# Performance work log

Hardware: AMD Instinct MI355X
Metric: run time of the kernel (lower is better)

## Reference

```python
import jax, jax.numpy as jnp
import numpy as np

NUM_CLASSES = 1024
KERNEL_MUL = 2.0
KERNEL_NUM = 5


def setup_inputs() -> dict:
    key = jax.random.key(0)
    k1, k2, k3 = jax.random.split(key, 3)
    N, D = 131072, 256
    x_rgb = jax.random.normal(k1, (N, D), dtype=jnp.float32)
    x_ir = jax.random.normal(k2, (N, D), dtype=jnp.float32)
    targets = jax.random.randint(k3, (N,), 0, NUM_CLASSES, dtype=jnp.int64)
    return {"x_rgb": x_rgb, "x_ir": x_ir, "targets": targets}


def _centers_by_id(x_rgb, x_ir, targets):
    # groupby-mean: one-pass segment sum + count (replaces the python loop)
    ones = jnp.ones(targets.shape, dtype=x_rgb.dtype)
    counts = jax.ops.segment_sum(ones, targets, num_segments=NUM_CLASSES)
    denom = jnp.maximum(counts, 1.0)[:, None]
    c_rgb = jax.ops.segment_sum(x_rgb, targets, num_segments=NUM_CLASSES) / denom
    c_ir = jax.ops.segment_sum(x_ir, targets, num_segments=NUM_CLASSES) / denom
    return c_rgb, c_ir  # [C, D] each


def _gaussian_kernel(total):
    # pairwise squared distances via ||a||^2 + ||b||^2 - 2 a.b (no NxNxD tensor)
    sq = jnp.sum(total * total, axis=1)
    dists = sq[:, None] + sq[None, :] - 2.0 * (total @ total.T)
    dists = jnp.maximum(dists, 0.0)  # fp-safety; exact form is nonnegative
    n = total.shape[0]
    # bandwidth computed on detached dists (matches `dists.data`)
    bandwidth = jax.lax.stop_gradient(jnp.sum(dists)) / (n * n - n)
    bandwidth = bandwidth / (KERNEL_MUL ** (KERNEL_NUM // 2))
    kernels = sum(
        jnp.exp(-dists / (bandwidth * (KERNEL_MUL ** i))) for i in range(KERNEL_NUM)
    )
    return kernels


def reference(x_rgb, x_ir, targets):
    c_rgb, c_ir = _centers_by_id(x_rgb, x_ir, targets)
    B = c_rgb.shape[0]
    total = jnp.concatenate([c_rgb, c_ir], axis=0)  # [2C, D]
    kernels = _gaussian_kernel(total)
    XX = kernels[:B, :B]
    YY = kernels[B:, B:]
    XY = kernels[:B, B:]
    YX = kernels[B:, :B]
    loss = jnp.mean(XX + YY - XY - YX)
    return loss
```

## Files before the change

### kernel.cpp

```cpp
#include <hip/hip_runtime.h>

#define NCLS 1024
#define DIM  256
#define NTOT 2048
#define CAP  256

__device__ __forceinline__ float4 f4add(float4 a, float4 b){
  return make_float4(a.x+b.x, a.y+b.y, a.z+b.z, a.w+b.w);
}

__global__ void k_init(int* cursor){
  cursor[threadIdx.x] = 0;
}

__global__ __launch_bounds__(256) void k_scatter(const int* __restrict__ tgt, int n,
                                                 int* __restrict__ cursor,
                                                 int* __restrict__ index){
  for (int i = blockIdx.x*blockDim.x + threadIdx.x; i < n; i += gridDim.x*blockDim.x){
    int t = tgt[i];
    int pos = atomicAdd(&cursor[t], 1);
    if (pos < CAP) index[t*CAP + pos] = i;
  }
}

__global__ __launch_bounds__(256) void k_gather(const float* __restrict__ xr,
    const float* __restrict__ xi, const int* __restrict__ index,
    const int* __restrict__ cursor, float* __restrict__ Ppart)
{
  int bid = blockIdx.x;
  int cls = bid >> 2;
  int h   = (bid >> 1) & 1;
  int a   = bid & 1;
  int tid = threadIdx.x;
  int l = tid & 63, g = tid >> 6;
  int cnt = cursor[cls]; if (cnt > CAP) cnt = CAP;
  int off = cls*CAP;
  int c0 = (cnt + 1) >> 1;
  int start = off + (h ? c0 : 0);
  int end   = off + (h ? cnt : c0);
  const float4* __restrict__ X4 = (const float4*)(a ? xi : xr);

  float4 s0 = make_float4(0,0,0,0), s1 = make_float4(0,0,0,0);
  int j = start + g;
  for (; j + 4 < end; j += 8){
    unsigned r0 = (unsigned)index[j];
    unsigned r1 = (unsigned)index[j+4];
    float4 v0 = X4[r0*64u + l];
    float4 v1 = X4[r1*64u + l];
    s0 = f4add(s0, v0);
    s1 = f4add(s1, v1);
  }
  if (j < end) s0 = f4add(s0, X4[(unsigned)index[j]*64u + l]);
  s0 = f4add(s0, s1);

  __shared__ float4 sh[256];
  sh[tid] = s0; __syncthreads();
  if (tid < 64){
    float4 r = f4add(f4add(sh[tid], sh[tid+64]), f4add(sh[tid+128], sh[tid+192]));
    ((float4*)Ppart)[bid*64 + tid] = r;
  }
}

__global__ __launch_bounds__(256) void k_combine(const float* __restrict__ Ppart,
    const int* __restrict__ cursor, float* __restrict__ T, float* __restrict__ sq)
{
  int wv  = blockIdx.x*4 + (threadIdx.x >> 6);
  int cls = wv >> 1, a = wv & 1;
  int l   = threadIdx.x & 63;
  const float4* P4 = (const float4*)Ppart;
  float4 p0 = P4[(cls*4 + 0 + a)*64 + l];
  float4 p1 = P4[(cls*4 + 2 + a)*64 + l];
  int cnt = cursor[cls]; if (cnt > CAP) cnt = CAP;
  float invd = 1.f / fmaxf((float)cnt, 1.f);
  float4 c;
  c.x = (p0.x + p1.x) * invd;
  c.y = (p0.y + p1.y) * invd;
  c.z = (p0.z + p1.z) * invd;
  c.w = (p0.w + p1.w) * invd;
  int row = a ? (NCLS + cls) : cls;
  ((float4*)T)[row*64 + l] = c;
  float v = c.x*c.x + c.y*c.y + c.z*c.z + c.w*c.w;
  #pragma unroll
  for (int o = 32; o > 0; o >>= 1) v += __shfl_down(v, o);
  if (l == 0) sq[row] = v;
}

__global__ __launch_bounds__(256) void k_colsum(const float* __restrict__ T,
                                                float* __restrict__ Pcol){
  int b = blockIdx.x;
  int tid = threadIdx.x;
  int l = tid & 63, g = tid >> 6;
  const float4* T4 = (const float4*)T;
  float4 acc = make_float4(0,0,0,0);
  for (int r = b*64 + g; r < b*64 + 64; r += 4)
    acc = f4add(acc, T4[r*64 + l]);
  __shared__ float4 sh[256];
  sh[tid] = acc; __syncthreads();
  if (tid < 64){
    float4 r = f4add(f4add(sh[tid], sh[tid+64]), f4add(sh[tid+128], sh[tid+192]));
    ((float4*)Pcol)[b*64 + tid] = r;
  }
}

__global__ __launch_bounds__(256) void k_bw(const float* __restrict__ sq,
    const float* __restrict__ Pcol, float* __restrict__ invbw,
    double* __restrict__ lossacc){
  int t = threadIdx.x;
  double acc = 0.0;
  for (int i = t; i < NTOT; i += 256) acc += (double)sq[i];
  float cs = 0.f;
  for (int b = 0; b < 32; ++b) cs += Pcol[b*DIM + t];
  double c2 = (double)cs * (double)cs;
  #pragma unroll
  for (int o = 32; o > 0; o >>= 1){
    acc += __shfl_down(acc, o);
    c2  += __shfl_down(c2, o);
  }
  __shared__ double ra[4], rc[4];
  int lane = t & 63, wid = t >> 6;
  if (lane == 0){ ra[wid] = acc; rc[wid] = c2; }
  __syncthreads();
  if (t == 0){
    double S_sq = ra[0]+ra[1]+ra[2]+ra[3];
    double S_cs = rc[0]+rc[1]+rc[2]+rc[3];
    double S1 = 2.0*(double)NTOT*S_sq - 2.0*S_cs;
    double bw = S1 / ((double)NTOT*(double)NTOT - (double)NTOT) / 4.0;
    #pragma unroll
    for (int k = 0; k < 5; ++k)
      invbw[k] = (float)(1.0 / (bw * (double)(1 << k)));
    *lossacc = 0.0;
  }
}

__global__ __launch_bounds__(256) void k_mmd(const float* __restrict__ T,
    const float* __restrict__ sq, const float* __restrict__ invbw,
    double* __restrict__ lossacc)
{
  int bx = blockIdx.x, by = blockIdx.y;
  if (bx < by) return;
  __shared__ float AsT[64][68];
  __shared__ float BsT[64][68];
  __shared__ float red[4];
  int tid = threadIdx.x;
  int tx = tid & 15, ty = tid >> 4;
  int rowA = by*64, rowB = bx*64;
  float acc[4][4];
  #pragma unroll
  for (int a = 0; a < 4; ++a)
    #pragma unroll
    for (int b = 0; b < 4; ++b) acc[a][b] = 0.f;

  for (int kk = 0; kk < DIM; kk += 64){
    #pragma unroll
    for (int it = 0; it < 4; ++it){
      int idx = it*256 + tid;
      int r = idx >> 4, c4 = idx & 15;
      float4 va = *(const float4*)&T[(rowA + r)*DIM + kk + c4*4];
      float4 vb = *(const float4*)&T[(rowB + r)*DIM + kk + c4*4];
      AsT[c4*4+0][r] = va.x; AsT[c4*4+1][r] = va.y;
      AsT[c4*4+2][r] = va.z; AsT[c4*4+3][r] = va.w;
      BsT[c4*4+0][r] = vb.x; BsT[c4*4+1][r] = vb.y;
      BsT[c4*4+2][r] = vb.z; BsT[c4*4+3][r] = vb.w;
    }
    __syncthreads();
    #pragma unroll 8
    for (int k = 0; k < 64; ++k){
      float4 av = *(const float4*)&AsT[k][ty*4];
      float4 bv = *(const float4*)&BsT[k][tx*4];
      acc[0][0] += av.x*bv.x; acc[0][1] += av.x*bv.y; acc[0][2] += av.x*bv.z; acc[0][3] += av.x*bv.w;
      acc[1][0] += av.y*bv.x; acc[1][1] += av.y*bv.y; acc[1][2] += av.y*bv.z; acc[1][3] += av.y*bv.w;
      acc[2][0] += av.z*bv.x; acc[2][1] += av.z*bv.y; acc[2][2] += av.z*bv.z; acc[2][3] += av.z*bv.w;
      acc[3][0] += av.w*bv.x; acc[3][1] += av.w*bv.y; acc[3][2] += av.w*bv.z; acc[3][3] += av.w*bv.w;
    }
    __syncthreads();
  }

  float i0 = invbw[0], i1 = invbw[1], i2 = invbw[2], i3 = invbw[3], i4 = invbw[4];
  float wgt = (bx > by) ? 2.f : 1.f;
  float lacc = 0.f;
  #pragma unroll
  for (int a = 0; a < 4; ++a){
    int i = rowA + ty*4 + a;
    float sqi  = sq[i];
    float sgnI = (i < NCLS) ? 1.f : -1.f;
    #pragma unroll
    for (int b = 0; b < 4; ++b){
      int j = rowB + tx*4 + b;
      float d = sqi + sq[j] - 2.f*acc[a][b];
      d = fmaxf(d, 0.f);
      float w = __expf(-d*i0) + __expf(-d*i1) + __expf(-d*i2) + __expf(-d*i3) + __expf(-d*i4);
      lacc += ((j < NCLS) ? sgnI : -sgnI) * w;
    }
  }
  lacc *= wgt;
  #pragma unroll
  for (int o = 32; o > 0; o >>= 1) lacc += __shfl_down(lacc, o);
  int lane = tid & 63, wid = tid >> 6;
  if (lane == 0) red[wid] = lacc;
  __syncthreads();
  if (tid == 0) atomicAdd(lossacc, (double)(red[0]+red[1]+red[2]+red[3]));
}

__global__ void k_final(const double* __restrict__ lossacc, float* __restrict__ out){
  out[0] = (float)(*lossacc * (1.0 / ((double)NCLS * (double)NCLS)));
}

extern "C" void kernel_launch(void* const* d_in, const int* in_sizes, int n_in,
                              void* d_out, int out_size, void* d_ws, size_t ws_size,
                              hipStream_t stream) {
  const float* xr  = (const float*)d_in[0];
  const float* xi  = (const float*)d_in[1];
  const int*   tgt = (const int*)d_in[2];
  float* out = (float*)d_out;
  int n = in_sizes[2];

  char* w = (char*)d_ws;
  int* cursor   = (int*)w;
  int* index    = cursor + NCLS;
  float* T      = (float*)(index + NCLS*CAP);
  float* sq     = T + NTOT*DIM;
  float* invbw  = sq + NTOT;
  double* lossd = (double*)(invbw + 8);
  float* Ppart  = (float*)(lossd + 1);
  float* Pcol   = Ppart + 4*NCLS*DIM;

  k_init<<<1, 1024, 0, stream>>>(cursor);
  k_scatter<<<256, 256, 0, stream>>>(tgt, n, cursor, index);
  k_gather<<<4*NCLS, 256, 0, stream>>>(xr, xi, index, cursor, Ppart);
  k_combine<<<NTOT/4, 256, 0, stream>>>(Ppart, cursor, T, sq);
  k_colsum<<<32, 256, 0, stream>>>(T, Pcol);
  k_bw<<<1, 256, 0, stream>>>(sq, Pcol, invbw, lossd);
  k_mmd<<<dim3(32, 32), 256, 0, stream>>>(T, sq, invbw, lossd);
  k_final<<<1, 1, 0, stream>>>(lossd, out);
}
```

Baseline: 135.1 us.

## Compute pairwise Gram tile with split-bf16 MFMA instead of scalar FP32 FMA

The combine kernel now also writes hi/lo bf16 splits of the centers matrix. The MMD kernel computes the 64x64 Gram tiles with three bf16 MFMA 16x16x32 products per k-step (hi*hi, hi*lo, lo*hi) in place of a scalar FP32 outer-product loop. This moves the matmul onto matrix cores while keeping close to FP32 accuracy. The cost is extra global writes for the split copies and a small precision loss from dropping the lo*lo term.

```diff
diff --git a/kernel.cpp b/kernel.cpp
--- a/kernel.cpp
+++ b/kernel.cpp
@@ -5,8 +5,18 @@
 #define NTOT 2048
 #define CAP  256
 
+typedef short bf16x8 __attribute__((ext_vector_type(8)));
+typedef float f32x4  __attribute__((ext_vector_type(4)));
+
 __device__ __forceinline__ float4 f4add(float4 a, float4 b){
   return make_float4(a.x+b.x, a.y+b.y, a.z+b.z, a.w+b.w);
+}
+__device__ __forceinline__ unsigned short f2bf(float x){
+  unsigned u = __float_as_uint(x);
+  return (unsigned short)((u + 0x7FFFu + ((u >> 16) & 1u)) >> 16);
+}
+__device__ __forceinline__ float bf2f(unsigned short h){
+  return __uint_as_float(((unsigned)h) << 16);
 }
 
 __global__ void k_init(int* cursor){
@@ -62,7 +72,9 @@
 }
 
 __global__ __launch_bounds__(256) void k_combine(const float* __restrict__ Ppart,
-    const int* __restrict__ cursor, float* __restrict__ T, float* __restrict__ sq)
+    const int* __restrict__ cursor, float* __restrict__ T,
+    unsigned short* __restrict__ Thi, unsigned short* __restrict__ Tlo,
+    float* __restrict__ sq)
 {
   int wv  = blockIdx.x*4 + (threadIdx.x >> 6);
   int cls = wv >> 1, a = wv & 1;
@@ -79,6 +91,13 @@
   c.w = (p0.w + p1.w) * invd;
   int row = a ? (NCLS + cls) : cls;
   ((float4*)T)[row*64 + l] = c;
+  ushort4 h4, l4;
+  h4.x = f2bf(c.x); l4.x = f2bf(c.x - bf2f(h4.x));
+  h4.y = f2bf(c.y); l4.y = f2bf(c.y - bf2f(h4.y));
+  h4.z = f2bf(c.z); l4.z = f2bf(c.z - bf2f(h4.z));
+  h4.w = f2bf(c.w); l4.w = f2bf(c.w - bf2f(h4.w));
+  *(ushort4*)&Thi[row*DIM + l*4] = h4;
+  *(ushort4*)&Tlo[row*DIM + l*4] = l4;
   float v = c.x*c.x + c.y*c.y + c.z*c.z + c.w*c.w;
   #pragma unroll
   for (int o = 32; o > 0; o >>= 1) v += __shfl_down(v, o);
@@ -132,71 +151,74 @@
   }
 }
 
-__global__ __launch_bounds__(256) void k_mmd(const float* __restrict__ T,
+__global__ __launch_bounds__(256) void k_mmd(
+    const unsigned short* __restrict__ Thi, const unsigned short* __restrict__ Tlo,
     const float* __restrict__ sq, const float* __restrict__ invbw,
     double* __restrict__ lossacc)
 {
   int bx = blockIdx.x, by = blockIdx.y;
   if (bx < by) return;
-  __shared__ float AsT[64][68];
-  __shared__ float BsT[64][68];
+  __shared__ unsigned short Ah[64][40], Al[64][40], Bh[64][40], Bl[64][40];
   __shared__ float red[4];
   int tid = threadIdx.x;
-  int tx = tid & 15, ty = tid >> 4;
+  int w = tid >> 6, l = tid & 63;
   int rowA = by*64, rowB = bx*64;
-  float acc[4][4];
-  #pragma unroll
-  for (int a = 0; a < 4; ++a)
+  f32x4 acc[4];
+  #pragma unroll
+  for (int t = 0; t < 4; ++t) acc[t] = (f32x4){0.f,0.f,0.f,0.f};
+
+  int srow = tid >> 2, sseg = (tid & 3)*8;
+  int ar = w*16 + (l & 15);
+  int kg = (l >> 4)*8;
+
+  for (int kk = 0; kk < DIM; kk += 32){
+    __syncthreads();
+    *(bf16x8*)&Ah[srow][sseg] = *(const bf16x8*)&Thi[(rowA+srow)*DIM + kk + sseg];
+    *(bf16x8*)&Al[srow][sseg] = *(const bf16x8*)&Tlo[(rowA+srow)*DIM + kk + sseg];
+    *(bf16x8*)&Bh[srow][sseg] = *(const bf16x8*)&Thi[(rowB+srow)*DIM + kk + sseg];
+    *(bf16x8*)&Bl[srow][sseg] = *(const bf16x8*)&Tlo[(rowB+srow)*DIM + kk + sseg];
+    __syncthreads();
+    bf16x8 ah = *(const bf16x8*)&Ah[ar][kg];
+    bf16x8 al = *(const bf16x8*)&Al[ar][kg];
     #pragma unroll
-    for (int b = 0; b < 4; ++b) acc[a][b] = 0.f;
-
-  for (int kk = 0; kk < DIM; kk += 64){
-    #pragma unroll
-    for (int it = 0; it < 4; ++it){
-      int idx = it*256 + tid;
-      int r = idx >> 4, c4 = idx & 15;
-      float4 va = *(const float4*)&T[(rowA + r)*DIM + kk + c4*4];
-      float4 vb = *(const float4*)&T[(rowB + r)*DIM + kk + c4*4];
-      AsT[c4*4+0][r] = va.x; AsT[c4*4+1][r] = va.y;
-      AsT[c4*4+2][r] = va.z; AsT[c4*4+3][r] = va.w;
-      BsT[c4*4+0][r] = vb.x; BsT[c4*4+1][r] = vb.y;
-      BsT[c4*4+2][r] = vb.z; BsT[c4*4+3][r] = vb.w;
+    for (int t = 0; t < 4; ++t){
+      int br = t*16 + (l & 15);
+      bf16x8 bh = *(const bf16x8*)&Bh[br][kg];
+      bf16x8 bl = *(const bf16x8*)&Bl[br][kg];
+      acc[t] = __builtin_amdgcn_mfma_f32_16x16x32_bf16(ah, bh, acc[t], 0, 0, 0);
+      acc[t] = __builtin_amdgcn_mfma_f32_16x16x32_bf16(ah, bl, acc[t], 0, 0, 0);
+      acc[t] = __builtin_amdgcn_mfma_f32_16x16x32_bf16(al, bh, acc[t], 0, 0, 0);
     }
-    __syncthreads();
-    #pragma unroll 8
-    for (int k = 0; k < 64; ++k){
-      float4 av = *(const float4*)&AsT[k][ty*4];
-      float4 bv = *(const float4*)&BsT[k][tx*4];
-      acc[0][0] += av.x*bv.x; acc[0][1] += av.x*bv.y; acc[0][2] += av.x*bv.z; acc[0][3] += av.x*bv.w;
-      acc[1][0] += av.y*bv.x; acc[1][1] += av.y*bv.y; acc[1][2] += av.y*bv.z; acc[1][3] += av.y*bv.w;
-      acc[2][0] += av.z*bv.x; acc[2][1] += av.z*bv.y; acc[2][2] += av.z*bv.z; acc[2][3] += av.z*bv.w;
-      acc[3][0] += av.w*bv.x; acc[3][1] += av.w*bv.y; acc[3][2] += av.w*bv.z; acc[3][3] += av.w*bv.w;
-    }
-    __syncthreads();
   }
 
   float i0 = invbw[0], i1 = invbw[1], i2 = invbw[2], i3 = invbw[3], i4 = invbw[4];
   float wgt = (bx > by) ? 2.f : 1.f;
   float lacc = 0.f;
-  #pragma unroll
-  for (int a = 0; a < 4; ++a){
-    int i = rowA + ty*4 + a;
-    float sqi  = sq[i];
-    float sgnI = (i < NCLS) ? 1.f : -1.f;
+  int ibase = rowA + w*16 + ((l >> 4)*4);
+  float sqi[4]; float sgnI[4];
+  #pragma unroll
+  for (int r = 0; r < 4; ++r){
+    int i = ibase + r;
+    sqi[r]  = sq[i];
+    sgnI[r] = (i < NCLS) ? 1.f : -1.f;
+  }
+  #pragma unroll
+  for (int t = 0; t < 4; ++t){
+    int j = rowB + t*16 + (l & 15);
+    float sqj = sq[j];
+    bool jn = (j < NCLS);
     #pragma unroll
-    for (int b = 0; b < 4; ++b){
-      int j = rowB + tx*4 + b;
-      float d = sqi + sq[j] - 2.f*acc[a][b];
+    for (int r = 0; r < 4; ++r){
+      float d = sqi[r] + sqj - 2.f*acc[t][r];
       d = fmaxf(d, 0.f);
-      float w = __expf(-d*i0) + __expf(-d*i1) + __expf(-d*i2) + __expf(-d*i3) + __expf(-d*i4);
-      lacc += ((j < NCLS) ? sgnI : -sgnI) * w;
+      float ws = __expf(-d*i0) + __expf(-d*i1) + __expf(-d*i2) + __expf(-d*i3) + __expf(-d*i4);
+      lacc += (jn ? sgnI[r] : -sgnI[r]) * ws;
     }
   }
   lacc *= wgt;
   #pragma unroll
   for (int o = 32; o > 0; o >>= 1) lacc += __shfl_down(lacc, o);
-  int lane = tid & 63, wid = tid >> 6;
-  if (lane == 0) red[wid] = lacc;
+  if (l == 0) red[w] = lacc;
   __syncthreads();
   if (tid == 0) atomicAdd(lossacc, (double)(red[0]+red[1]+red[2]+red[3]));
 }
@@ -223,13 +245,15 @@
   double* lossd = (double*)(invbw + 8);
   float* Ppart  = (float*)(lossd + 1);
   float* Pcol   = Ppart + 4*NCLS*DIM;
+  unsigned short* Thi = (unsigned short*)(Pcol + 32*DIM);
+  unsigned short* Tlo = Thi + NTOT*DIM;
 
   k_init<<<1, 1024, 0, stream>>>(cursor);
   k_scatter<<<256, 256, 0, stream>>>(tgt, n, cursor, index);
   k_gather<<<4*NCLS, 256, 0, stream>>>(xr, xi, index, cursor, Ppart);
-  k_combine<<<NTOT/4, 256, 0, stream>>>(Ppart, cursor, T, sq);
+  k_combine<<<NTOT/4, 256, 0, stream>>>(Ppart, cursor, T, Thi, Tlo, sq);
   k_colsum<<<32, 256, 0, stream>>>(T, Pcol);
   k_bw<<<1, 256, 0, stream>>>(sq, Pcol, invbw, lossd);
-  k_mmd<<<dim3(32, 32), 256, 0, stream>>>(T, sq, invbw, lossd);
+  k_mmd<<<dim3(32, 32), 256, 0, stream>>>(Thi, Tlo, sq, invbw, lossd);
   k_final<<<1, 1, 0, stream>>>(lossd, out);
 }
```

Measured after the change: 116.9 us. -13.5%, faster.
